# Kernel tuning notes

Measured on AMD Instinct MI355X. Metric: run time of the kernel, lower is better.

The kernel has to match this reference:

```python
import jax, jax.numpy as jnp
import numpy as np
import math

EMBED_DIM = 256
NUM_HEADS = 32
D_K = EMBED_DIM // NUM_HEADS  # 8 qubits per head circuit


def setup_inputs() -> dict:
    key = jax.random.key(0)
    k1, k2, k3, k4 = jax.random.split(key, 4)
    B, S = 2, 2048
    x = jax.random.normal(k1, (B, S, EMBED_DIM), dtype=jnp.float32)
    mask = jnp.ones((B, S), dtype=jnp.int32)
    # trainable RX angles, one per wire, shared across heads (single _QLayer instance)
    theta = jax.random.normal(k2, (D_K,), dtype=jnp.float32)
    # out_proj Linear(embed_dim, embed_dim) with bias
    bound = 1.0 / math.sqrt(EMBED_DIM)
    W_out = jax.random.uniform(k3, (EMBED_DIM, EMBED_DIM), dtype=jnp.float32, minval=-bound, maxval=bound)
    b_out = jax.random.uniform(k4, (EMBED_DIM,), dtype=jnp.float32, minval=-bound, maxval=bound)
    return {"x": x, "mask": mask, "theta": theta, "W_out": W_out, "b_out": b_out}


def reference(x, mask, theta, W_out, b_out):
    B, S, E = x.shape
    H, dk = NUM_HEADS, D_K
    # [B, H, S, d_k]
    xh = x.reshape(B, S, H, dk).transpose(0, 2, 1, 3)
    # Quantum circuit per element: RX(x) then RX(theta) on |0>, measure PauliZ.
    # Product state => <Z_i> = cos(x_i + theta_i). Exact closed form.
    q = jnp.cos(xh + theta)  # [B, H, S, dk]
    scores = jnp.einsum('bhqd,bhkd->bhqk', q, q) / jnp.float32(math.sqrt(dk))
    scores = jnp.where(mask[:, None, None, :] == 0, jnp.float32(-1e9), scores)
    attn = jax.nn.softmax(scores, axis=-1)  # dropout is identity in eval mode
    out = jnp.einsum('bhqk,bhkd->bhqd', attn, q)
    out = out.transpose(0, 2, 1, 3).reshape(B, S, E)
    return out @ W_out.T + b_out
```

## Files before the change

### kernel.cpp

```cpp
#include <hip/hip_runtime.h>

#define B_ 2
#define S_ 2048
#define E_ 256
#define H_ 32
#define DK_ 8

typedef float f32x4 __attribute__((ext_vector_type(4)));
typedef short short8 __attribute__((ext_vector_type(8)));
typedef unsigned short us8 __attribute__((ext_vector_type(8)));

#define SQ_ 0.71419638f
#define CONES_F 0.71484375f
#define CONES_BITS 0x3F373F37u
#define CORR_ (CONES_F / SQ_)

static __device__ __forceinline__ float ex2(float x) {
#if __has_builtin(__builtin_amdgcn_exp2f)
  return __builtin_amdgcn_exp2f(x);
#else
  float r; asm("v_exp_f32 %0, %1\n\ts_nop 0" : "=v"(r) : "v"(x)); return r;
#endif
}

static __device__ __forceinline__ unsigned cvtpk(float lo, float hi) {
  unsigned r;
  asm("v_cvt_pk_bf16_f32 %0, %1, %2" : "=v"(r) : "v"(lo), "v"(hi));
  return r;
}

__global__ __launch_bounds__(256) void qgen4(
    const float* __restrict__ x, const float* __restrict__ theta,
    unsigned short* __restrict__ qb) {
  __shared__ unsigned short TL[8][264];

  const int tid = threadIdx.x;
  const int gs = blockIdx.x * 8;
  const int b = gs >> 11, s0 = gs & (S_ - 1);

  float th[8];
#pragma unroll
  for (int d = 0; d < 8; ++d) th[d] = theta[d];

#pragma unroll
  for (int p = 0; p < 2; ++p) {
    int fi = tid + p * 256;
    int row = fi >> 6, col4 = fi & 63;
    float4 v = *(const float4*)&x[((size_t)(b * S_ + s0 + row)) * E_ + col4 * 4];
    int dbase = (col4 & 1) * 4;
    uint2 wv;
    wv.x = cvtpk(__cosf(v.x + th[dbase + 0]) * SQ_,
                 __cosf(v.y + th[dbase + 1]) * SQ_);
    wv.y = cvtpk(__cosf(v.z + th[dbase + 2]) * SQ_,
                 __cosf(v.w + th[dbase + 3]) * SQ_);
    *(uint2*)&TL[row][col4 * 4] = wv;
  }
  __syncthreads();

  const int h = tid >> 3, r = tid & 7;
  uint4 t = *(uint4*)&TL[r][h * 8];
  *(uint4*)&qb[((size_t)(b * H_ + h) * S_ + s0 + r) * DK_] = t;
}

__global__ __launch_bounds__(256) void attn4(
    const unsigned short* __restrict__ qb, const int* __restrict__ mask,
    float* __restrict__ ao) {
  __shared__ float4 K4[1024];
  __shared__ unsigned short KTs[DK_ * 1040];
  __shared__ unsigned Mk[512];
  __shared__ int sOK[4];

  const int bh = blockIdx.x >> 4;
  const int qblk = (blockIdx.x & 15) * 128;
  const int b = bh >> 5, h = bh & 31;
  const int tid = threadIdx.x;
  const int wid = tid >> 6, lane = tid & 63;
  const int c = lane & 15, g = lane >> 4;

  const float4 zero4 = make_float4(0.f, 0.f, 0.f, 0.f);
  uint4 cpat; cpat.x = CONES_BITS; cpat.y = CONES_BITS;
  cpat.z = CONES_BITS; cpat.w = CONES_BITS;

  const float4* qbv = (const float4*)(qb + (size_t)bh * S_ * DK_);

  const int qrow0 = qblk + wid * 32;
  short8 qf[2];
  f32x4 acc[2];
#pragma unroll
  for (int qt = 0; qt < 2; ++qt) {
    float4 t = zero4;
    if (lane < 16) t = qbv[qrow0 + qt * 16 + lane];
    qf[qt] = __builtin_bit_cast(short8, t);
    acc[qt] = (f32x4){0.f, 0.f, 0.f, 0.f};
  }

  const f32x4 zf = {0.f, 0.f, 0.f, 0.f};

#define KLOOP(MASKED)                                                        \
  for (int kt = 0; kt < 32; ++kt) {                                          \
    float4 a0f = K4[kt * 32 + c];                                            \
    float4 a1f = K4[kt * 32 + 16 + c];                                       \
    float4 vtf;                                                              \
    if (c < 8)       vtf = *(const float4*)&KTs[c * 1040 + kt * 32 + 8 * g]; \
    else if (c == 8) vtf = __builtin_bit_cast(float4, cpat);                 \
    else             vtf = zero4;                                            \
    uint2 mA, mB;                                                            \
    if (MASKED) {                                                            \
      mA = *(const uint2*)&Mk[kt * 16 + 2 * g];                              \
      mB = *(const uint2*)&Mk[kt * 16 + 8 + 2 * g];                          \
    }                                                                        \
    short8 aK0 = __builtin_bit_cast(short8, a0f);                            \
    short8 aK1 = __builtin_bit_cast(short8, a1f);                            \
    short8 aV  = __builtin_bit_cast(short8, vtf);                            \
    _Pragma("unroll")                                                        \
    for (int qt = 0; qt < 2; ++qt) {                                         \
      f32x4 s0 = __builtin_amdgcn_mfma_f32_16x16x32_bf16(aK0, qf[qt], zf, 0, 0, 0); \
      f32x4 s1 = __builtin_amdgcn_mfma_f32_16x16x32_bf16(aK1, qf[qt], zf, 0, 0, 0); \
      unsigned w0 = cvtpk(ex2(s0[0]), ex2(s0[1]));                           \
      unsigned w1 = cvtpk(ex2(s0[2]), ex2(s0[3]));                           \
      unsigned w2 = cvtpk(ex2(s1[0]), ex2(s1[1]));                           \
      unsigned w3 = cvtpk(ex2(s1[2]), ex2(s1[3]));                           \
      if (MASKED) { w0 &= mA.x; w1 &= mA.y; w2 &= mB.x; w3 &= mB.y; }        \
      asm("v_permlane32_swap_b32 %0, %1" : "+v"(w0), "+v"(w2));              \
      asm("v_permlane16_swap_b32 %0, %1" : "+v"(w0), "+v"(w2));              \
      asm("v_permlane32_swap_b32 %0, %1" : "+v"(w1), "+v"(w3));              \
      asm("v_permlane16_swap_b32 %0, %1" : "+v"(w1), "+v"(w3));              \
      uint4 pu; pu.x = w0; pu.y = w1; pu.z = w2; pu.w = w3;                  \
      acc[qt] = __builtin_amdgcn_mfma_f32_16x16x32_bf16(                     \
          aV, __builtin_bit_cast(short8, pu), acc[qt], 0, 0, 0);             \
    }                                                                        \
  }

#pragma unroll 1
  for (int p = 0; p < 2; ++p) {
    if (p) __syncthreads();
    const float4* src = qbv + p * 1024;
#pragma unroll
    for (int it = 0; it < 2; ++it) {
      int rp = tid + it * 256;
      int s = rp * 2;
      float4 f0 = src[s], f1 = src[s + 1];
      K4[s] = f0; K4[s + 1] = f1;
      us8 u0 = __builtin_bit_cast(us8, f0);
      us8 u1 = __builtin_bit_cast(us8, f1);
#pragma unroll
      for (int d = 0; d < 8; ++d) {
        unsigned wv = (unsigned)u0[d] | ((unsigned)u1[d] << 16);
        *(unsigned*)&KTs[d * 1040 + s] = wv;
      }
    }
    const int* mp = mask + b * S_ + p * 1024;
    int4 mv = *(const int4*)&mp[tid * 4];
    int ok = (mv.x != 0) & (mv.y != 0) & (mv.z != 0) & (mv.w != 0);
    Mk[2 * tid]     = (mv.x ? 0xFFFFu : 0u) | (mv.y ? 0xFFFF0000u : 0u);
    Mk[2 * tid + 1] = (mv.z ? 0xFFFFu : 0u) | (mv.w ? 0xFFFF0000u : 0u);
    int wall = __all(ok);
    if (lane == 0) sOK[wid] = wall;
    __syncthreads();
    int allones = sOK[0] & sOK[1] & sOK[2] & sOK[3];

    if (allones) { KLOOP(0) } else { KLOOP(1) }
  }
#undef KLOOP

#pragma unroll
  for (int qt = 0; qt < 2; ++qt) {
    float den = __shfl(acc[qt][0], 32 + c);
    float rd = CORR_ / den;
    if (g < 2) {
      int qrow = qrow0 + qt * 16 + c;
      float4 o;
      o.x = acc[qt][0] * rd; o.y = acc[qt][1] * rd;
      o.z = acc[qt][2] * rd; o.w = acc[qt][3] * rd;
      *(float4*)&ao[((size_t)(b * S_ + qrow)) * E_ + h * DK_ + g * 4] = o;
    }
  }
}

__global__ __launch_bounds__(256) void outproj2(
    const float* __restrict__ A, const float* __restrict__ W,
    const float* __restrict__ bias, float* __restrict__ C) {
  __shared__ float As[64][36];
  __shared__ float Ws[64][68];

  const int bm = blockIdx.x >> 2;
  const int bn = blockIdx.x & 3;
  const int tid = threadIdx.x;
  const int tm = tid >> 4, tn = tid & 15;
  const int m0 = tm * 2, n0 = tn * 4;

  float acc[2][4] = {};

  for (int kt = 0; kt < E_; kt += 64) {
#pragma unroll
    for (int f = 0; f < 2; ++f) {
      int fi = tid + f * 256;
      int row = fi >> 4;
      int kk = (fi & 15) << 2;
      float4 v = *(const float4*)&A[(size_t)(bm * 32 + row) * E_ + kt + kk];
      As[kk + 0][row] = v.x; As[kk + 1][row] = v.y;
      As[kk + 2][row] = v.z; As[kk + 3][row] = v.w;
    }
#pragma unroll
    for (int f = 0; f < 4; ++f) {
      int fi = tid + f * 256;
      int row = fi >> 4;
      int kk = (fi & 15) << 2;
      float4 wv = *(const float4*)&W[(size_t)(bn * 64 + row) * E_ + kt + kk];
      Ws[kk + 0][row] = wv.x; Ws[kk + 1][row] = wv.y;
      Ws[kk + 2][row] = wv.z; Ws[kk + 3][row] = wv.w;
    }
    __syncthreads();

#pragma unroll 8
    for (int kk = 0; kk < 64; ++kk) {
      float2 a = *(const float2*)&As[kk][m0];
      float4 w = *(const float4*)&Ws[kk][n0];
      float ar[2] = {a.x, a.y};
      float wr[4] = {w.x, w.y, w.z, w.w};
#pragma unroll
      for (int i = 0; i < 2; ++i)
#pragma unroll
        for (int j = 0; j < 4; ++j)
          acc[i][j] = fmaf(ar[i], wr[j], acc[i][j]);
    }
    __syncthreads();
  }

  float4 bv = *(const float4*)&bias[bn * 64 + n0];
  float br[4] = {bv.x, bv.y, bv.z, bv.w};
#pragma unroll
  for (int i = 0; i < 2; ++i) {
    int m = bm * 32 + m0 + i;
    float4 outv = make_float4(acc[i][0] + br[0], acc[i][1] + br[1],
                              acc[i][2] + br[2], acc[i][3] + br[3]);
    *(float4*)&C[(size_t)m * E_ + bn * 64 + n0] = outv;
  }
}

extern "C" void kernel_launch(void* const* d_in, const int* in_sizes, int n_in,
                              void* d_out, int out_size, void* d_ws, size_t ws_size,
                              hipStream_t stream) {
  const float* x     = (const float*)d_in[0];
  const int*   mask  = (const int*)d_in[1];
  const float* theta = (const float*)d_in[2];
  const float* W     = (const float*)d_in[3];
  const float* bvec  = (const float*)d_in[4];
  float* out = (float*)d_out;

  unsigned short* qbb = (unsigned short*)d_ws;
  float* ao = (float*)(qbb + (size_t)B_ * H_ * S_ * DK_);

  qgen4<<<512, 256, 0, stream>>>(x, theta, qbb);
  attn4<<<1024, 256, 0, stream>>>(qbb, mask, ao);
  outproj2<<<512, 256, 0, stream>>>(ao, W, bvec, out);
}
```

Measured before the change: 130.2 us.

## Fuse cosine feature generation into attention kernel and drop permlane swaps

Removes the separate qgen kernel: the attention kernel now reads x directly, computes the cosine features and bf16-packs them into shared memory for all 2048 keys at once, which eliminates the intermediate bf16 buffer round-trip and one launch. Each block now handles 256 queries (4 tiles per wave) over all keys in a single pass, with no mid-loop barrier. The V-transposed layout is permuted at store time so the permlane swaps in the inner loop can be dropped. In exchange, each block recomputes cosines for every key (8 blocks per head redo the same work), LDS use roughly doubles, and the grid shrinks to 512 blocks, which may lower occupancy.

```diff
diff --git a/kernel.cpp b/kernel.cpp
--- a/kernel.cpp
+++ b/kernel.cpp
@@ -5,10 +5,10 @@
 #define E_ 256
 #define H_ 32
 #define DK_ 8
+#define KTSTR 1036
 
 typedef float f32x4 __attribute__((ext_vector_type(4)));
 typedef short short8 __attribute__((ext_vector_type(8)));
-typedef unsigned short us8 __attribute__((ext_vector_type(8)));
 
 #define SQ_ 0.71419638f
 #define CONES_F 0.71484375f
@@ -19,7 +19,7 @@
 #if __has_builtin(__builtin_amdgcn_exp2f)
   return __builtin_amdgcn_exp2f(x);
 #else
-  float r; asm("v_exp_f32 %0, %1\n\ts_nop 0" : "=v"(r) : "v"(x)); return r;
+  float r; asm("v_exp_f32 %0, %1" : "=v"(r) : "v"(x)); return r;
 #endif
 }
 
@@ -29,142 +29,127 @@
   return r;
 }
 
-__global__ __launch_bounds__(256) void qgen4(
+__global__ __launch_bounds__(256) void attn5(
     const float* __restrict__ x, const float* __restrict__ theta,
-    unsigned short* __restrict__ qb) {
-  __shared__ unsigned short TL[8][264];
-
-  const int tid = threadIdx.x;
-  const int gs = blockIdx.x * 8;
-  const int b = gs >> 11, s0 = gs & (S_ - 1);
-
-  float th[8];
-#pragma unroll
-  for (int d = 0; d < 8; ++d) th[d] = theta[d];
-
-#pragma unroll
-  for (int p = 0; p < 2; ++p) {
-    int fi = tid + p * 256;
-    int row = fi >> 6, col4 = fi & 63;
-    float4 v = *(const float4*)&x[((size_t)(b * S_ + s0 + row)) * E_ + col4 * 4];
-    int dbase = (col4 & 1) * 4;
-    uint2 wv;
-    wv.x = cvtpk(__cosf(v.x + th[dbase + 0]) * SQ_,
-                 __cosf(v.y + th[dbase + 1]) * SQ_);
-    wv.y = cvtpk(__cosf(v.z + th[dbase + 2]) * SQ_,
-                 __cosf(v.w + th[dbase + 3]) * SQ_);
-    *(uint2*)&TL[row][col4 * 4] = wv;
-  }
-  __syncthreads();
-
-  const int h = tid >> 3, r = tid & 7;
-  uint4 t = *(uint4*)&TL[r][h * 8];
-  *(uint4*)&qb[((size_t)(b * H_ + h) * S_ + s0 + r) * DK_] = t;
-}
-
-__global__ __launch_bounds__(256) void attn4(
-    const unsigned short* __restrict__ qb, const int* __restrict__ mask,
-    float* __restrict__ ao) {
-  __shared__ float4 K4[1024];
-  __shared__ unsigned short KTs[DK_ * 1040];
-  __shared__ unsigned Mk[512];
+    const int* __restrict__ mask, float* __restrict__ ao) {
+  __shared__ float4 K4[S_];
+  __shared__ unsigned KTu[DK_ * KTSTR];
+  __shared__ unsigned Mk[S_ / 2];
   __shared__ int sOK[4];
 
-  const int bh = blockIdx.x >> 4;
-  const int qblk = (blockIdx.x & 15) * 128;
+  const int bh = blockIdx.x >> 3;
+  const int qblk = (blockIdx.x & 7) * 256;
   const int b = bh >> 5, h = bh & 31;
   const int tid = threadIdx.x;
   const int wid = tid >> 6, lane = tid & 63;
   const int c = lane & 15, g = lane >> 4;
 
-  const float4 zero4 = make_float4(0.f, 0.f, 0.f, 0.f);
-  uint4 cpat; cpat.x = CONES_BITS; cpat.y = CONES_BITS;
-  cpat.z = CONES_BITS; cpat.w = CONES_BITS;
-
-  const float4* qbv = (const float4*)(qb + (size_t)bh * S_ * DK_);
-
-  const int qrow0 = qblk + wid * 32;
-  short8 qf[2];
-  f32x4 acc[2];
-#pragma unroll
-  for (int qt = 0; qt < 2; ++qt) {
-    float4 t = zero4;
-    if (lane < 16) t = qbv[qrow0 + qt * 16 + lane];
-    qf[qt] = __builtin_bit_cast(short8, t);
+  const float* xb = x + (size_t)b * S_ * E_ + h * DK_;
+
+  float th[8];
+#pragma unroll
+  for (int d = 0; d < 8; ++d) th[d] = theta[d];
+
+  const int qrow0 = qblk + wid * 64;
+  short8 qf[4];
+  f32x4 acc[4];
+#pragma unroll
+  for (int qt = 0; qt < 4; ++qt) {
     acc[qt] = (f32x4){0.f, 0.f, 0.f, 0.f};
-  }
-
+    uint4 qq = {0u, 0u, 0u, 0u};
+    if (lane < 16) {
+      const float* xq = xb + (size_t)(qrow0 + qt * 16 + lane) * E_;
+      float4 a = *(const float4*)xq;
+      float4 bq = *(const float4*)(xq + 4);
+      qq.x = cvtpk(__cosf(a.x + th[0]) * SQ_, __cosf(a.y + th[1]) * SQ_);
+      qq.y = cvtpk(__cosf(a.z + th[2]) * SQ_, __cosf(a.w + th[3]) * SQ_);
+      qq.z = cvtpk(__cosf(bq.x + th[4]) * SQ_, __cosf(bq.y + th[5]) * SQ_);
+      qq.w = cvtpk(__cosf(bq.z + th[6]) * SQ_, __cosf(bq.w + th[7]) * SQ_);
+    }
+    qf[qt] = __builtin_bit_cast(short8, qq);
+  }
+
+  int okall = 1;
+#pragma unroll
+  for (int it = 0; it < 4; ++it) {
+    int pi = it * 256 + tid;
+    int s = pi * 2;
+    const float* xr = xb + (size_t)s * E_;
+    float4 v00 = *(const float4*)xr;
+    float4 v01 = *(const float4*)(xr + 4);
+    float4 v10 = *(const float4*)(xr + E_);
+    float4 v11 = *(const float4*)(xr + E_ + 4);
+    float c0[8], c1[8];
+    c0[0] = __cosf(v00.x + th[0]) * SQ_; c0[1] = __cosf(v00.y + th[1]) * SQ_;
+    c0[2] = __cosf(v00.z + th[2]) * SQ_; c0[3] = __cosf(v00.w + th[3]) * SQ_;
+    c0[4] = __cosf(v01.x + th[4]) * SQ_; c0[5] = __cosf(v01.y + th[5]) * SQ_;
+    c0[6] = __cosf(v01.z + th[6]) * SQ_; c0[7] = __cosf(v01.w + th[7]) * SQ_;
+    c1[0] = __cosf(v10.x + th[0]) * SQ_; c1[1] = __cosf(v10.y + th[1]) * SQ_;
+    c1[2] = __cosf(v10.z + th[2]) * SQ_; c1[3] = __cosf(v10.w + th[3]) * SQ_;
+    c1[4] = __cosf(v11.x + th[4]) * SQ_; c1[5] = __cosf(v11.y + th[5]) * SQ_;
+    c1[6] = __cosf(v11.z + th[6]) * SQ_; c1[7] = __cosf(v11.w + th[7]) * SQ_;
+    uint4 r0, r1;
+    r0.x = cvtpk(c0[0], c0[1]); r0.y = cvtpk(c0[2], c0[3]);
+    r0.z = cvtpk(c0[4], c0[5]); r0.w = cvtpk(c0[6], c0[7]);
+    r1.x = cvtpk(c1[0], c1[1]); r1.y = cvtpk(c1[2], c1[3]);
+    r1.z = cvtpk(c1[4], c1[5]); r1.w = cvtpk(c1[6], c1[7]);
+    K4[s]     = __builtin_bit_cast(float4, r0);
+    K4[s + 1] = __builtin_bit_cast(float4, r1);
+    int ktg = pi >> 4, m = pi & 15;
+    int w = 4 * ((m & 7) >> 1) + ((m >> 3) << 1) + (m & 1);
+    int base = ktg * 16 + w;
+#pragma unroll
+    for (int d = 0; d < 8; ++d)
+      KTu[d * KTSTR + base] = cvtpk(c0[d], c1[d]);
+
+    int2 mv = *(const int2*)&mask[b * S_ + s];
+    Mk[pi] = (mv.x ? 0xFFFFu : 0u) | (mv.y ? 0xFFFF0000u : 0u);
+    okall &= (mv.x != 0) & (mv.y != 0);
+  }
+  int wall = __all(okall);
+  if (lane == 0) sOK[wid] = wall;
+  __syncthreads();
+  const int allones = sOK[0] & sOK[1] & sOK[2] & sOK[3];
+
+  uint4 cpat = {CONES_BITS, CONES_BITS, CONES_BITS, CONES_BITS};
   const f32x4 zf = {0.f, 0.f, 0.f, 0.f};
-
-#define KLOOP(MASKED)                                                        \
-  for (int kt = 0; kt < 32; ++kt) {                                          \
-    float4 a0f = K4[kt * 32 + c];                                            \
-    float4 a1f = K4[kt * 32 + 16 + c];                                       \
-    float4 vtf;                                                              \
-    if (c < 8)       vtf = *(const float4*)&KTs[c * 1040 + kt * 32 + 8 * g]; \
-    else if (c == 8) vtf = __builtin_bit_cast(float4, cpat);                 \
-    else             vtf = zero4;                                            \
-    uint2 mA, mB;                                                            \
-    if (MASKED) {                                                            \
-      mA = *(const uint2*)&Mk[kt * 16 + 2 * g];                              \
-      mB = *(const uint2*)&Mk[kt * 16 + 8 + 2 * g];                          \
-    }                                                                        \
-    short8 aK0 = __builtin_bit_cast(short8, a0f);                            \
-    short8 aK1 = __builtin_bit_cast(short8, a1f);                            \
-    short8 aV  = __builtin_bit_cast(short8, vtf);                            \
-    _Pragma("unroll")                                                        \
-    for (int qt = 0; qt < 2; ++qt) {                                         \
+  const int vrow = (c & 7) * KTSTR;
+
+#define KLOOP(MASKED)                                                         \
+  _Pragma("unroll 2")                                                         \
+  for (int kt = 0; kt < 64; ++kt) {                                           \
+    float4 a0f = K4[kt * 32 + c];                                             \
+    float4 a1f = K4[kt * 32 + 16 + c];                                        \
+    uint4 vtu = *(const uint4*)&KTu[vrow + kt * 16 + 4 * g];                  \
+    if (c == 8) vtu = cpat;                                                   \
+    uint2 mA, mB;                                                             \
+    if (MASKED) {                                                             \
+      mA = *(const uint2*)&Mk[kt * 16 + 2 * g];                               \
+      mB = *(const uint2*)&Mk[kt * 16 + 8 + 2 * g];                           \
+    }                                                                         \
+    short8 aK0 = __builtin_bit_cast(short8, a0f);                             \
+    short8 aK1 = __builtin_bit_cast(short8, a1f);                             \
+    short8 aV  = __builtin_bit_cast(short8, vtu);                             \
+    _Pragma("unroll")                                                         \
+    for (int qt = 0; qt < 4; ++qt) {                                          \
       f32x4 s0 = __builtin_amdgcn_mfma_f32_16x16x32_bf16(aK0, qf[qt], zf, 0, 0, 0); \
       f32x4 s1 = __builtin_amdgcn_mfma_f32_16x16x32_bf16(aK1, qf[qt], zf, 0, 0, 0); \
-      unsigned w0 = cvtpk(ex2(s0[0]), ex2(s0[1]));                           \
-      unsigned w1 = cvtpk(ex2(s0[2]), ex2(s0[3]));                           \
-      unsigned w2 = cvtpk(ex2(s1[0]), ex2(s1[1]));                           \
-      unsigned w3 = cvtpk(ex2(s1[2]), ex2(s1[3]));                           \
-      if (MASKED) { w0 &= mA.x; w1 &= mA.y; w2 &= mB.x; w3 &= mB.y; }        \
-      asm("v_permlane32_swap_b32 %0, %1" : "+v"(w0), "+v"(w2));              \
-      asm("v_permlane16_swap_b32 %0, %1" : "+v"(w0), "+v"(w2));              \
-      asm("v_permlane32_swap_b32 %0, %1" : "+v"(w1), "+v"(w3));              \
-      asm("v_permlane16_swap_b32 %0, %1" : "+v"(w1), "+v"(w3));              \
-      uint4 pu; pu.x = w0; pu.y = w1; pu.z = w2; pu.w = w3;                  \
-      acc[qt] = __builtin_amdgcn_mfma_f32_16x16x32_bf16(                     \
-          aV, __builtin_bit_cast(short8, pu), acc[qt], 0, 0, 0);             \
-    }                                                                        \
-  }
-
-#pragma unroll 1
-  for (int p = 0; p < 2; ++p) {
-    if (p) __syncthreads();
-    const float4* src = qbv + p * 1024;
-#pragma unroll
-    for (int it = 0; it < 2; ++it) {
-      int rp = tid + it * 256;
-      int s = rp * 2;
-      float4 f0 = src[s], f1 = src[s + 1];
-      K4[s] = f0; K4[s + 1] = f1;
-      us8 u0 = __builtin_bit_cast(us8, f0);
-      us8 u1 = __builtin_bit_cast(us8, f1);
-#pragma unroll
-      for (int d = 0; d < 8; ++d) {
-        unsigned wv = (unsigned)u0[d] | ((unsigned)u1[d] << 16);
-        *(unsigned*)&KTs[d * 1040 + s] = wv;
-      }
-    }
-    const int* mp = mask + b * S_ + p * 1024;
-    int4 mv = *(const int4*)&mp[tid * 4];
-    int ok = (mv.x != 0) & (mv.y != 0) & (mv.z != 0) & (mv.w != 0);
-    Mk[2 * tid]     = (mv.x ? 0xFFFFu : 0u) | (mv.y ? 0xFFFF0000u : 0u);
-    Mk[2 * tid + 1] = (mv.z ? 0xFFFFu : 0u) | (mv.w ? 0xFFFF0000u : 0u);
-    int wall = __all(ok);
-    if (lane == 0) sOK[wid] = wall;
-    __syncthreads();
-    int allones = sOK[0] & sOK[1] & sOK[2] & sOK[3];
-
-    if (allones) { KLOOP(0) } else { KLOOP(1) }
-  }
+      unsigned w0 = cvtpk(ex2(s0[0]), ex2(s0[1]));                            \
+      unsigned w1 = cvtpk(ex2(s0[2]), ex2(s0[3]));                            \
+      unsigned w2 = cvtpk(ex2(s1[0]), ex2(s1[1]));                            \
+      unsigned w3 = cvtpk(ex2(s1[2]), ex2(s1[3]));                            \
+      if (MASKED) { w0 &= mA.x; w1 &= mA.y; w2 &= mB.x; w3 &= mB.y; }         \
+      uint4 pu; pu.x = w0; pu.y = w1; pu.z = w2; pu.w = w3;                   \
+      acc[qt] = __builtin_amdgcn_mfma_f32_16x16x32_bf16(                      \
+          aV, __builtin_bit_cast(short8, pu), acc[qt], 0, 0, 0);              \
+    }                                                                         \
+  }
+
+  if (allones) { KLOOP(0) } else { KLOOP(1) }
 #undef KLOOP
 
 #pragma unroll
-  for (int qt = 0; qt < 2; ++qt) {
+  for (int qt = 0; qt < 4; ++qt) {
     float den = __shfl(acc[qt][0], 32 + c);
     float rd = CORR_ / den;
     if (g < 2) {
@@ -248,10 +233,8 @@
   const float* bvec  = (const float*)d_in[4];
   float* out = (float*)d_out;
 
-  unsigned short* qbb = (unsigned short*)d_ws;
-  float* ao = (float*)(qbb + (size_t)B_ * H_ * S_ * DK_);
-
-  qgen4<<<512, 256, 0, stream>>>(x, theta, qbb);
-  attn4<<<1024, 256, 0, stream>>>(qbb, mask, ao);
+  float* ao = (float*)d_ws;
+
+  attn5<<<B_ * H_ * 8, 256, 0, stream>>>(x, theta, mask, ao);
   outproj2<<<512, 256, 0, stream>>>(ao, W, bvec, out);
 }
```

Result: faster. 126.0 us (-3.3%).
